# Kernel tuning notes

Hardware: AMD Instinct MI355X
Metric: run time of the kernel (lower is better)

The kernel has to match this reference:

```python
import jax, jax.numpy as jnp
import numpy as np

RRELU_SLOPE = (1.0 / 8.0 + 1.0 / 3.0) / 2.0  # RReLU eval-mode negative slope


def _layer(h, edge_feats, src, dst, W, b, Lw, Lb, n_nodes):
    # per-edge message: concat(src node feat, edge feat) -> linear
    msg = jnp.concatenate([h[src], edge_feats], axis=-1) @ W + b  # [E, H]
    # mean-aggregate messages by destination node (0 for isolated nodes, DGL semantics)
    s = jax.ops.segment_sum(msg, dst, num_segments=n_nodes)  # [N, H]
    cnt = jax.ops.segment_sum(jnp.ones((dst.shape[0], 1), msg.dtype), dst,
                              num_segments=n_nodes)  # [N, 1]
    agg = jnp.where(cnt > 0, s / jnp.maximum(cnt, 1.0), 0.0)
    # self-loop linear add
    agg = agg + h @ Lw + Lb
    # RReLU (eval mode = leaky relu with slope (lower+upper)/2); dropout p=0 is identity
    return jnp.where(agg >= 0, agg, agg * RRELU_SLOPE)


def setup_inputs() -> dict:
    key = jax.random.key(0)
    ks = jax.random.split(key, 12)
    N, E, D, H = 50000, 640000, 128, 128
    sc_in = 1.0 / np.sqrt(2 * D)
    sc_d = 1.0 / np.sqrt(D)
    sc_o = 1.0 / np.sqrt(2 * H)
    return {
        "node_feats": jax.random.normal(ks[0], (N, D), jnp.float32),
        "edge_feats": jax.random.normal(ks[1], (E, D), jnp.float32),
        "src": jax.random.randint(ks[2], (E,), 0, N),
        "dst": jax.random.randint(ks[3], (E,), 0, N),
        "W1": jax.random.uniform(ks[4], (2 * D, H), jnp.float32, -sc_in, sc_in),
        "b1": jnp.zeros((H,), jnp.float32),
        "L1": jax.random.uniform(ks[5], (D, H), jnp.float32, -sc_d, sc_d),
        "lb1": jnp.zeros((H,), jnp.float32),
        "W2": jax.random.uniform(ks[6], (2 * H, H), jnp.float32, -sc_in, sc_in),
        "b2": jnp.zeros((H,), jnp.float32),
        "L2": jax.random.uniform(ks[7], (H, H), jnp.float32, -sc_d, sc_d),
        "lb2": jnp.zeros((H,), jnp.float32),
        "Wo": jax.random.uniform(ks[8], (2 * H, H), jnp.float32, -sc_o, sc_o),
        "bo": jnp.zeros((H,), jnp.float32),
    }


def reference(node_feats, edge_feats, src, dst, W1, b1, L1, lb1, W2, b2, L2, lb2, Wo, bo):
    n = node_feats.shape[0]
    h1 = _layer(node_feats, edge_feats, src, dst, W1, b1, L1, lb1, n)
    h2 = _layer(h1, edge_feats, src, dst, W2, b2, L2, lb2, n)
    multihop = jnp.concatenate([h1, h2], axis=-1)  # [N, 2H]
    return multihop @ Wo + bo
```

## Files before the change

### kernel.cpp

```cpp
#include <hip/hip_runtime.h>
#include <hip/hip_bf16.h>

typedef unsigned short u16;
typedef unsigned int   u32;

using bf16x8 = __attribute__((ext_vector_type(8))) __bf16;
using f32x4  = __attribute__((ext_vector_type(4))) float;

#define SLOPE 0.22916666666666666f
#define CAP 64

static __device__ __forceinline__ u16 f2bf(float f) {
    u32 u = __float_as_uint(f);
    u += 0x7fffu + ((u >> 16) & 1u);
    return (u16)(u >> 16);
}
static __device__ __forceinline__ float bf2f(u16 h) {
    return __uint_as_float(((u32)h) << 16);
}

static __device__ __forceinline__ void gload_lds16(const u16* g, u16* l) {
    __builtin_amdgcn_global_load_lds(
        (const __attribute__((address_space(1))) void*)g,
        (__attribute__((address_space(3))) void*)l,
        16, 0, 0);
}

static __device__ __forceinline__ void add8(float* a, uint4 u) {
    a[0] += bf2f((u16)u.x); a[1] += bf2f((u16)(u.x >> 16));
    a[2] += bf2f((u16)u.y); a[3] += bf2f((u16)(u.y >> 16));
    a[4] += bf2f((u16)u.z); a[5] += bf2f((u16)(u.z >> 16));
    a[6] += bf2f((u16)u.w); a[7] += bf2f((u16)(u.w >> 16));
}

__global__ void k_prep(const int* __restrict__ src, const int* __restrict__ dst,
                       int* __restrict__ deg, int2* __restrict__ se,
                       const float* __restrict__ node, u16* __restrict__ nfb,
                       const float* __restrict__ W1, const float* __restrict__ L1,
                       const float* __restrict__ W2, const float* __restrict__ L2,
                       const float* __restrict__ Wo, u16* __restrict__ T,
                       int E, int n8, int gE, int gF) {
    int b = blockIdx.x, t = threadIdx.x;
    if (b < gE) {
        int i = b * 256 + t;
        if (i < E) {
            int d = dst[i];
            int p = atomicAdd(&deg[d], 1);
            if (p < CAP) se[(size_t)d * CAP + p] = make_int2(src[i], i);
        }
    } else if (b < gE + gF) {
        int i = (b - gE) * 256 + t;
        if (i < n8) {
            const float4* p = (const float4*)node + (size_t)i * 2;
            float4 a = p[0], c = p[1];
            union { u16 u[8]; uint4 v; } pk;
            pk.u[0] = f2bf(a.x); pk.u[1] = f2bf(a.y); pk.u[2] = f2bf(a.z); pk.u[3] = f2bf(a.w);
            pk.u[4] = f2bf(c.x); pk.u[5] = f2bf(c.y); pk.u[6] = f2bf(c.z); pk.u[7] = f2bf(c.w);
            *((uint4*)nfb + i) = pk.v;
        }
    } else {
        int m = b - gE - gF;
        const float* S; int rowoff;
        switch (m) {
            case 0: S = W1; rowoff = 0;   break;
            case 1: S = W1; rowoff = 128; break;
            case 2: S = L1; rowoff = 0;   break;
            case 3: S = W2; rowoff = 0;   break;
            case 4: S = W2; rowoff = 128; break;
            case 5: S = L2; rowoff = 0;   break;
            case 6: S = Wo; rowoff = 0;   break;
            default: S = Wo; rowoff = 128; break;
        }
        u16* O = T + m * 16384;
        for (int i = t; i < 16384; i += 256) {
            int c = i >> 7, k = i & 127;
            O[i] = f2bf(S[(rowoff + k) * 128 + c]);
        }
    }
}

__global__ void k_aggf(const float* __restrict__ ef, const u16* __restrict__ nfb,
                       const int2* __restrict__ se, const int* __restrict__ deg,
                       u16* __restrict__ EF, u16* __restrict__ A, int N) {
    int w = (blockIdx.x * blockDim.x + threadIdx.x) >> 6;
    int lane = threadIdx.x & 63;
    if (w >= N) return;
    int t4 = lane >> 4, qq = lane & 15;
    int d = deg[w];
    int dc = d < CAP ? d : CAP;
    const int2* sp = se + (size_t)w * CAP;
    float e[8] = {0.f, 0.f, 0.f, 0.f, 0.f, 0.f, 0.f, 0.f};
    float n[8] = {0.f, 0.f, 0.f, 0.f, 0.f, 0.f, 0.f, 0.f};
    int i = 0;
    for (; i + 8 <= dc; i += 8) {
        int2 iA = sp[i + t4], iB = sp[i + 4 + t4];
        const float* ra = ef + (size_t)iA.y * 128 + qq * 8;
        const float* rb = ef + (size_t)iB.y * 128 + qq * 8;
        float4 a0 = *(const float4*)ra, a1 = *(const float4*)(ra + 4);
        float4 c0 = *(const float4*)rb, c1 = *(const float4*)(rb + 4);
        uint4 ua = *(const uint4*)(nfb + (size_t)iA.x * 128 + qq * 8);
        uint4 ub = *(const uint4*)(nfb + (size_t)iB.x * 128 + qq * 8);
        e[0] += a0.x + c0.x; e[1] += a0.y + c0.y; e[2] += a0.z + c0.z; e[3] += a0.w + c0.w;
        e[4] += a1.x + c1.x; e[5] += a1.y + c1.y; e[6] += a1.z + c1.z; e[7] += a1.w + c1.w;
        add8(n, ua); add8(n, ub);
    }
    for (; i + 4 <= dc; i += 4) {
        int2 iA = sp[i + t4];
        const float* ra = ef + (size_t)iA.y * 128 + qq * 8;
        float4 a0 = *(const float4*)ra, a1 = *(const float4*)(ra + 4);
        uint4 ua = *(const uint4*)(nfb + (size_t)iA.x * 128 + qq * 8);
        e[0] += a0.x; e[1] += a0.y; e[2] += a0.z; e[3] += a0.w;
        e[4] += a1.x; e[5] += a1.y; e[6] += a1.z; e[7] += a1.w;
        add8(n, ua);
    }
    if (i + t4 < dc) {
        int2 iA = sp[i + t4];
        const float* ra = ef + (size_t)iA.y * 128 + qq * 8;
        float4 a0 = *(const float4*)ra, a1 = *(const float4*)(ra + 4);
        uint4 ua = *(const uint4*)(nfb + (size_t)iA.x * 128 + qq * 8);
        e[0] += a0.x; e[1] += a0.y; e[2] += a0.z; e[3] += a0.w;
        e[4] += a1.x; e[5] += a1.y; e[6] += a1.z; e[7] += a1.w;
        add8(n, ua);
    }
    #pragma unroll
    for (int j = 0; j < 8; j++) {
        e[j] += __shfl_xor(e[j], 16); e[j] += __shfl_xor(e[j], 32);
        n[j] += __shfl_xor(n[j], 16); n[j] += __shfl_xor(n[j], 32);
    }
    float sc = d > 0 ? 1.0f / (float)d : 0.0f;
    if (t4 == 0) {
        union { u16 u[8]; uint4 v; } pk;
        #pragma unroll
        for (int j = 0; j < 8; j++) pk.u[j] = f2bf(e[j] * sc);
        *(uint4*)(EF + (size_t)w * 128 + qq * 8) = pk.v;
    } else if (t4 == 1) {
        union { u16 u[8]; uint4 v; } pk;
        #pragma unroll
        for (int j = 0; j < 8; j++) pk.u[j] = f2bf(n[j] * sc);
        *(uint4*)(A + (size_t)w * 128 + qq * 8) = pk.v;
    }
}

__global__ void k_aggb(const u16* __restrict__ h, const int2* __restrict__ se,
                       const int* __restrict__ deg, u16* __restrict__ out, int N) {
    int w = (blockIdx.x * blockDim.x + threadIdx.x) >> 6;
    int lane = threadIdx.x & 63;
    if (w >= N) return;
    int quarter = lane >> 4, q = lane & 15;
    int d = deg[w];
    int dc = d < CAP ? d : CAP;
    const int2* sp = se + (size_t)w * CAP;
    float a[8] = {0.f, 0.f, 0.f, 0.f, 0.f, 0.f, 0.f, 0.f};
    int i = 0;
    for (; i + 8 <= dc; i += 8) {
        int eA = sp[i + quarter].x, eB = sp[i + 4 + quarter].x;
        uint4 uA = *(const uint4*)(h + (size_t)eA * 128 + q * 8);
        uint4 uB = *(const uint4*)(h + (size_t)eB * 128 + q * 8);
        add8(a, uA); add8(a, uB);
    }
    for (; i + 4 <= dc; i += 4) {
        int eA = sp[i + quarter].x;
        uint4 uA = *(const uint4*)(h + (size_t)eA * 128 + q * 8);
        add8(a, uA);
    }
    if (i + quarter < dc) {
        int eA = sp[i + quarter].x;
        uint4 uA = *(const uint4*)(h + (size_t)eA * 128 + q * 8);
        add8(a, uA);
    }
    #pragma unroll
    for (int j = 0; j < 8; j++) {
        a[j] += __shfl_xor(a[j], 32);
        a[j] += __shfl_xor(a[j], 16);
    }
    if (quarter == 0) {
        float sc = d > 0 ? 1.0f / (float)d : 0.0f;
        union { u16 u[8]; uint4 v; } pk;
        #pragma unroll
        for (int j = 0; j < 8; j++) pk.u[j] = f2bf(a[j] * sc);
        *(uint4*)(out + (size_t)w * 128 + q * 8) = pk.v;
    }
}

#define STAGE_X128(LBUF, GPTR)                                                      \
    {                                                                               \
        _Pragma("unroll")                                                           \
        for (int i_ = 0; i_ < 4; i_++) {                                            \
            int id_ = t + i_ * 512;                                                 \
            int r_ = id_ >> 4, c16_ = id_ & 15;                                     \
            int rg_ = row0 + r_; if (rg_ >= N) rg_ = N - 1;                         \
            gload_lds16((GPTR) + (size_t)rg_ * 128 + ((c16_ ^ (r_ & 15)) << 3),     \
                        (LBUF) + id_ * 8);                                          \
        }                                                                           \
    }
#define STAGE_W512(GPTR)                                                            \
    {                                                                               \
        _Pragma("unroll")                                                           \
        for (int i_ = 0; i_ < 4; i_++) {                                            \
            int id_ = t + i_ * 512;                                                 \
            int cc_ = id_ >> 4, c16_ = id_ & 15;                                    \
            gload_lds16((GPTR) + cc_ * 128 + ((c16_ ^ (cc_ & 15)) << 3),            \
                        Wl + id_ * 8);                                              \
        }                                                                           \
    }
#define COMPUTE(LBUF)                                                               \
    {                                                                               \
        _Pragma("unroll")                                                           \
        for (int ks_ = 0; ks_ < 4; ks_++) {                                         \
            bf16x8 af_[2], bf_[4];                                                  \
            _Pragma("unroll")                                                       \
            for (int h_ = 0; h_ < 2; h_++) {                                        \
                int r_ = wr * 32 + h_ * 16 + lanelo;                                \
                int ch_ = (ks_ * 4 + lanehi) ^ (r_ & 15);                           \
                af_[h_] = *(const bf16x8*)((LBUF) + r_ * 128 + ch_ * 8);            \
            }                                                                       \
            _Pragma("unroll")                                                       \
            for (int g_ = 0; g_ < 4; g_++) {                                        \
                int cc_ = wc * 64 + g_ * 16 + lanelo;                               \
                int ch_ = (ks_ * 4 + lanehi) ^ (cc_ & 15);                          \
                bf_[g_] = *(const bf16x8*)(Wl + cc_ * 128 + ch_ * 8);               \
            }                                                                       \
            _Pragma("unroll")                                                       \
            for (int h_ = 0; h_ < 2; h_++)                                          \
                _Pragma("unroll")                                                   \
                for (int g_ = 0; g_ < 4; g_++)                                      \
                    acc[h_][g_] = __builtin_amdgcn_mfma_f32_16x16x32_bf16(          \
                        af_[h_], bf_[g_], acc[h_][g_], 0, 0, 0);                    \
        }                                                                           \
    }

__global__ __launch_bounds__(512, 4) void k_gemm3s(
    const u16* __restrict__ X0, const u16* __restrict__ X1, const u16* __restrict__ X2,
    const u16* __restrict__ T0, const u16* __restrict__ T1, const u16* __restrict__ T2,
    const float* __restrict__ bm, const int* __restrict__ deg,
    const float* __restrict__ ba, u16* __restrict__ outp, int N) {

    __shared__ u16 XB[128 * 128];
    __shared__ u16 Wl[128 * 128];

    int t = threadIdx.x, lane = t & 63, wid = t >> 6;
    int lanelo = lane & 15, lanehi = lane >> 4;
    int wr = wid >> 1, wc = wid & 1;
    int row0 = blockIdx.x * 128;

    f32x4 acc[2][4];
    #pragma unroll
    for (int h = 0; h < 2; h++)
        #pragma unroll
        for (int g = 0; g < 4; g++) acc[h][g] = (f32x4){0.f, 0.f, 0.f, 0.f};

    STAGE_X128(XB, X0);
    STAGE_W512(T0);
    __syncthreads();
    COMPUTE(XB);
    __syncthreads();
    STAGE_X128(XB, X1);
    STAGE_W512(T1);
    __syncthreads();
    COMPUTE(XB);
    __syncthreads();
    STAGE_X128(XB, X2);
    STAGE_W512(T2);
    __syncthreads();
    COMPUTE(XB);

    #pragma unroll
    for (int h = 0; h < 2; h++) {
        #pragma unroll
        for (int r = 0; r < 4; r++) {
            int rowt = wr * 32 + h * 16 + lanehi * 4 + r;
            int rg = row0 + rowt;
            if (rg >= N) continue;
            float m = (deg[rg] > 0) ? 1.f : 0.f;
            #pragma unroll
            for (int g = 0; g < 4; g++) {
                int col = wc * 64 + g * 16 + lanelo;
                float v = acc[h][g][r] + ba[col] + m * bm[col];
                v = (v >= 0.f) ? v : v * SLOPE;
                outp[(size_t)rg * 128 + col] = f2bf(v);
            }
        }
    }
}

__global__ __launch_bounds__(512, 4) void k_gemmo(
    const u16* __restrict__ X0, const u16* __restrict__ X1,
    const u16* __restrict__ T0, const u16* __restrict__ T1,
    const float* __restrict__ ba, float* __restrict__ outp, int N) {

    __shared__ u16 XB[128 * 128];
    __shared__ u16 Wl[128 * 128];

    int t = threadIdx.x, lane = t & 63, wid = t >> 6;
    int lanelo = lane & 15, lanehi = lane >> 4;
    int wr = wid >> 1, wc = wid & 1;
    int row0 = blockIdx.x * 128;

    f32x4 acc[2][4];
    #pragma unroll
    for (int h = 0; h < 2; h++)
        #pragma unroll
        for (int g = 0; g < 4; g++) acc[h][g] = (f32x4){0.f, 0.f, 0.f, 0.f};

    STAGE_X128(XB, X0);
    STAGE_W512(T0);
    __syncthreads();
    COMPUTE(XB);
    __syncthreads();
    STAGE_X128(XB, X1);
    STAGE_W512(T1);
    __syncthreads();
    COMPUTE(XB);

    #pragma unroll
    for (int h = 0; h < 2; h++) {
        #pragma unroll
        for (int r = 0; r < 4; r++) {
            int rowt = wr * 32 + h * 16 + lanehi * 4 + r;
            int rg = row0 + rowt;
            if (rg >= N) continue;
            #pragma unroll
            for (int g = 0; g < 4; g++) {
                int col = wc * 64 + g * 16 + lanelo;
                outp[(size_t)rg * 128 + col] = acc[h][g][r] + ba[col];
            }
        }
    }
}


extern "C" void kernel_launch(void* const* d_in, const int* in_sizes, int n_in,
                              void* d_out, int out_size, void* d_ws, size_t ws_size,
                              hipStream_t stream) {
    const float* node = (const float*)d_in[0];
    const float* ef   = (const float*)d_in[1];
    const int*   src  = (const int*)d_in[2];
    const int*   dst  = (const int*)d_in[3];
    const float* W1   = (const float*)d_in[4];
    const float* b1   = (const float*)d_in[5];
    const float* L1   = (const float*)d_in[6];
    const float* lb1  = (const float*)d_in[7];
    const float* W2   = (const float*)d_in[8];
    const float* b2   = (const float*)d_in[9];
    const float* L2   = (const float*)d_in[10];
    const float* lb2  = (const float*)d_in[11];
    const float* Wo   = (const float*)d_in[12];
    const float* bo   = (const float*)d_in[13];
    int N = in_sizes[0] / 128;
    int E = in_sizes[2];

    char* ws = (char*)d_ws;
    size_t o = 0;
    auto alloc = [&](size_t bytes) {
        void* p = ws + o;
        o = (o + bytes + 511) & ~(size_t)511;
        return p;
    };
    int*  deg = (int*)alloc((size_t)N * 4);
    int2* se  = (int2*)alloc((size_t)N * CAP * 8);
    u16*  T   = (u16*)alloc((size_t)8 * 16384 * 2);
    u16*  nfb = (u16*)alloc((size_t)N * 128 * 2);
    u16*  EF  = (u16*)alloc((size_t)N * 128 * 2);
    u16*  A   = (u16*)alloc((size_t)N * 128 * 2);
    u16*  h1  = (u16*)alloc((size_t)N * 128 * 2);
    u16*  h2  = (u16*)alloc((size_t)N * 128 * 2);

    hipMemsetAsync(deg, 0, (size_t)N * 4, stream);

    int gE = (E + 255) / 256;
    int n8 = N * 128 / 8;
    int gF = (n8 + 255) / 256;
    k_prep<<<gE + gF + 8, 256, 0, stream>>>(src, dst, deg, se, node, nfb,
                                            W1, L1, W2, L2, Wo, T, E, n8, gE, gF);

    int gA = (N + 3) / 4;
    k_aggf<<<gA, 256, 0, stream>>>(ef, nfb, se, deg, EF, A, N);

    int gb = (N + 127) / 128;
    k_gemm3s<<<gb, 512, 0, stream>>>(A, EF, nfb, T, T + 16384, T + 2 * 16384,
                                     b1, deg, lb1, h1, N);
    k_aggb<<<gA, 256, 0, stream>>>(h1, se, deg, A, N);
    k_gemm3s<<<gb, 512, 0, stream>>>(A, EF, h1, T + 3 * 16384, T + 4 * 16384, T + 5 * 16384,
                                     b2, deg, lb2, h2, N);
    k_gemmo<<<gb, 512, 0, stream>>>(h1, h2, T + 6 * 16384, T + 7 * 16384,
                                    bo, (float*)d_out, N);
}
```

Baseline: 203.4 us.

## Partition edge bucketing by destination range and split weight transpose across blocks

The edge-bucketing phase now launches eight blocks per 512-edge chunk, each handling only destinations in one eighth of the node range. On MI355X, whose blocks are spread round-robin over eight XCDs, this is meant to keep each deg/se region's atomics and writes local to one XCD's L2. The weight transpose is also split from 8 blocks into 64 blocks of 2048 elements each, shortening that tail. In exchange, every fill block reads each dst value eight times, and the locality benefit depends on the hardware's block-to-XCD mapping.

```diff
diff --git a/kernel.cpp b/kernel.cpp
--- a/kernel.cpp
+++ b/kernel.cpp
@@ -39,17 +39,26 @@
                        const float* __restrict__ W1, const float* __restrict__ L1,
                        const float* __restrict__ W2, const float* __restrict__ L2,
                        const float* __restrict__ Wo, u16* __restrict__ T,
-                       int E, int n8, int gE, int gF) {
+                       int E, int N, int n8, int gFill, int gF) {
     int b = blockIdx.x, t = threadIdx.x;
-    if (b < gE) {
-        int i = b * 256 + t;
-        if (i < E) {
-            int d = dst[i];
-            int p = atomicAdd(&deg[d], 1);
-            if (p < CAP) se[(size_t)d * CAP + p] = make_int2(src[i], i);
-        }
-    } else if (b < gE + gF) {
-        int i = (b - gE) * 256 + t;
+    if (b < gFill) {
+        int chunk = b >> 3, g = b & 7;
+        int lo = (int)(((long long)g * N) >> 3);
+        int hi = (int)(((long long)(g + 1) * N) >> 3);
+        int base = chunk * 512;
+        #pragma unroll
+        for (int k = 0; k < 2; k++) {
+            int i = base + k * 256 + t;
+            if (i < E) {
+                int d = dst[i];
+                if (d >= lo && d < hi) {
+                    int p = atomicAdd(&deg[d], 1);
+                    if (p < CAP) se[(size_t)d * CAP + p] = make_int2(src[i], i);
+                }
+            }
+        }
+    } else if (b < gFill + gF) {
+        int i = (b - gFill) * 256 + t;
         if (i < n8) {
             const float4* p = (const float4*)node + (size_t)i * 2;
             float4 a = p[0], c = p[1];
@@ -59,7 +68,8 @@
             *((uint4*)nfb + i) = pk.v;
         }
     } else {
-        int m = b - gE - gF;
+        int mb = b - gFill - gF;
+        int m = mb >> 3, chunk = mb & 7;
         const float* S; int rowoff;
         switch (m) {
             case 0: S = W1; rowoff = 0;   break;
@@ -72,9 +82,10 @@
             default: S = Wo; rowoff = 128; break;
         }
         u16* O = T + m * 16384;
-        for (int i = t; i < 16384; i += 256) {
-            int c = i >> 7, k = i & 127;
-            O[i] = f2bf(S[(rowoff + k) * 128 + c]);
+        int j0 = chunk * 2048, j1 = j0 + 2048;
+        for (int j = j0 + t; j < j1; j += 256) {
+            int c = j >> 7, k = j & 127;
+            O[j] = f2bf(S[(rowoff + k) * 128 + c]);
         }
     }
 }
@@ -367,11 +378,13 @@
 
     hipMemsetAsync(deg, 0, (size_t)N * 4, stream);
 
-    int gE = (E + 255) / 256;
+    int nChunk = (E + 511) / 512;
+    int gFill = nChunk * 8;
     int n8 = N * 128 / 8;
     int gF = (n8 + 255) / 256;
-    k_prep<<<gE + gF + 8, 256, 0, stream>>>(src, dst, deg, se, node, nfb,
-                                            W1, L1, W2, L2, Wo, T, E, n8, gE, gF);
+    k_prep<<<gFill + gF + 64, 256, 0, stream>>>(src, dst, deg, se, node, nfb,
+                                                W1, L1, W2, L2, Wo, T,
+                                                E, N, n8, gFill, gF);
 
     int gA = (N + 3) / 4;
     k_aggf<<<gA, 256, 0, stream>>>(ef, nfb, se, deg, EF, A, N);
```

After: 195.2 us. 1.04x faster.
